# Optimization experiments

Measured on AMD Instinct MI355X. Metric: run time of the kernel, lower is better.

The kernel has to match this reference:

```python
import jax, jax.numpy as jnp
import numpy as np

N_HEADS = 8

def setup_inputs() -> dict:
    key = jax.random.key(0)
    k1, k2, k3 = jax.random.split(key, 3)
    B, T, C = 16, 1024, 512
    x = jax.random.normal(k1, (B, T, C), dtype=jnp.float32)
    Wqkv = jax.random.normal(k2, (C, 3 * C), dtype=jnp.float32) * (1.0 / np.sqrt(C))
    Wout = jax.random.normal(k3, (C, C), dtype=jnp.float32) * (1.0 / np.sqrt(C))
    return {"x": x, "Wqkv": Wqkv, "Wout": Wout}

def reference(x, Wqkv, Wout):
    B, T, C = x.shape
    H = N_HEADS
    Dh = C // H
    scale = 1.0 / (Dh ** 0.5)
    # qkv projection: [B,T,3,H,Dh] -> q,k,v each [B,H,T,Dh]
    qkv = (x @ Wqkv).reshape(B, T, 3, H, Dh)
    q = jnp.transpose(qkv[:, :, 0], (0, 2, 1, 3))
    k = jnp.transpose(qkv[:, :, 1], (0, 2, 1, 3))
    v = jnp.transpose(qkv[:, :, 2], (0, 2, 1, 3))
    att = jnp.einsum('bhqd,bhkd->bhqk', q, k) * scale  # [B,H,T,T]
    causal = jnp.tril(jnp.ones((T, T), dtype=bool))
    att = jnp.where(causal, att, -jnp.inf)
    att = jax.nn.softmax(att, axis=-1)
    y = jnp.einsum('bhqk,bhkd->bhqd', att, v)  # [B,H,T,Dh]
    y = jnp.transpose(y, (0, 2, 1, 3)).reshape(B, T, C)
    return y @ Wout
```

## Files before the change

kernel.cpp:

```cpp
#include <hip/hip_runtime.h>
#include <hip/hip_bf16.h>

typedef __bf16 bf16;
typedef __bf16 bf16x4 __attribute__((ext_vector_type(4)));
typedef __bf16 bf16x8 __attribute__((ext_vector_type(8)));
typedef float  f32x4  __attribute__((ext_vector_type(4)));

#define BB 16
#define TT 1024
#define CC 512
#define HH 8
#define DH 64

#define QSCALE 0.18033688011112042f
#define RESCALE_THR 10.0f

__device__ __forceinline__ void gload16(const void* gsrc, void* ldst) {
    __builtin_amdgcn_global_load_lds(
        (const __attribute__((address_space(1))) void*)gsrc,
        (__attribute__((address_space(3))) void*)ldst, 16, 0, 0);
}

__device__ __forceinline__ f32x4 mfma16(bf16x8 a, bf16x8 b, f32x4 c) {
    return __builtin_amdgcn_mfma_f32_16x16x32_bf16(a, b, c, 0, 0, 0);
}

__global__ __launch_bounds__(256)
void k_prep(const float* __restrict__ x, const float* __restrict__ wqkv,
            const float* __restrict__ wout,
            bf16* __restrict__ xb, bf16* __restrict__ wqt, bf16* __restrict__ wot)
{
    const int stride = gridDim.x * blockDim.x;
    const int i0 = blockIdx.x * blockDim.x + threadIdx.x;
    const int NX4 = BB * TT * CC / 4;
    for (int i = i0; i < NX4; i += stride) {
        float4 v = *(const float4*)(x + (size_t)i * 4);
        bf16x4 o = { (bf16)v.x, (bf16)v.y, (bf16)v.z, (bf16)v.w };
        *(bf16x4*)(xb + (size_t)i * 4) = o;
    }
    const int NQ = CC * 3 * CC;
    for (int i = i0; i < NQ; i += stride) {
        int k = i / (3 * CC), n = i - k * (3 * CC);
        wqt[(size_t)n * CC + k] = (bf16)wqkv[i];
    }
    const int NO = CC * CC;
    for (int i = i0; i < NO; i += stride) {
        int k = i / CC, n = i - k * CC;
        wot[(size_t)n * CC + k] = (bf16)wout[i];
    }
}

__global__ __launch_bounds__(512)
void k_attn(const bf16* __restrict__ qg, const bf16* __restrict__ kg,
            const bf16* __restrict__ vtg, bf16* __restrict__ yb)
{
    __shared__ __align__(16) bf16 sK[2][32 * 72];
    __shared__ __align__(16) bf16 sV[2][64 * 40];
    __shared__ __align__(16) bf16 sP[8][16 * 40];
    const int tid = threadIdx.x, w = tid >> 6, lane = tid & 63;
    const int l15 = lane & 15, l4 = lane >> 4;

    const int bid = blockIdx.x;
    const int xcd = bid & 7;
    const int j   = bid >> 3;
    const int bh  = xcd * 16 + (j >> 2);
    const int qp  = j & 3;

    const bf16* Q  = qg  + (size_t)bh * TT * DH;
    const bf16* Kp = kg  + (size_t)bh * TT * DH;
    const bf16* Vt = vtg + (size_t)bh * DH * TT;
    const int b = bh >> 3, h = bh & 7;

    const bool kstage = (tid < 256);
    const int ks_row = tid >> 3;
    const int ks_col = (tid & 7) * 8;
    const int t2 = tid & 255;
    const int vs_row = t2 >> 2;
    const int vs_col = (t2 & 3) * 8;

    bf16* myP = &sP[w][0];
    const f32x4 zero = {0.f, 0.f, 0.f, 0.f};

    for (int up = 0; up < 2; ++up) {
        const int qblk = up ? (7 - qp) : qp;
        const int qb   = qblk * 128 + w * 16;
        const int nt   = (qblk + 1) * 4;

        bf16x8 qf[2];
#pragma unroll
        for (int kk = 0; kk < 2; ++kk)
            qf[kk] = *(const bf16x8*)(Q + (size_t)(qb + l15) * DH + kk * 32 + l4 * 8);

        f32x4 y[4];
        float m_ = -1e30f, lp_ = 0.f;
#pragma unroll
        for (int dj = 0; dj < 4; ++dj) y[dj] = zero;

        if (kstage) {
            uint4 k0 = *(const uint4*)(Kp + (size_t)ks_row * DH + ks_col);
            *(uint4*)(&sK[0][ks_row * 72 + ks_col]) = k0;
        } else {
            uint4 v0 = *(const uint4*)(Vt + (size_t)vs_row * TT + vs_col);
            *(uint4*)(&sV[0][vs_row * 40 + vs_col]) = v0;
        }
        __syncthreads();

        for (int t = 0; t < nt; ++t) {
            const int t0 = t * 32;
            const int cur = t & 1, nxt = cur ^ 1;
            const bool more = (t + 1 < nt);
            uint4 sreg;
            if (more) {
                sreg = kstage
                    ? *(const uint4*)(Kp + (size_t)(t0 + 32 + ks_row) * DH + ks_col)
                    : *(const uint4*)(Vt + (size_t)vs_row * TT + t0 + 32 + vs_col);
            }

            if (t0 < qb + 16) {
                bf16x8 kf[2][2];
#pragma unroll
                for (int nj = 0; nj < 2; ++nj) {
                    const int row = nj * 16 + l15;
#pragma unroll
                    for (int kk = 0; kk < 2; ++kk)
                        kf[nj][kk] = *(const bf16x8*)(&sK[cur][row * 72 + ((kk << 2) | l4) * 8]);
                }
                f32x4 s[2];
#pragma unroll
                for (int nj = 0; nj < 2; ++nj) {
                    f32x4 a = mfma16(kf[nj][0], qf[0], zero);
                    s[nj] = mfma16(kf[nj][1], qf[1], a);
                }
                if (t0 + 32 > qb) {
#pragma unroll
                    for (int nj = 0; nj < 2; ++nj)
#pragma unroll
                        for (int rg = 0; rg < 4; ++rg)
                            if (t0 + nj * 16 + l4 * 4 + rg > qb + l15)
                                s[nj][rg] = -1e30f;
                }
                float mx = fmaxf(fmaxf(fmaxf(s[0][0], s[0][1]), fmaxf(s[0][2], s[0][3])),
                                 fmaxf(fmaxf(s[1][0], s[1][1]), fmaxf(s[1][2], s[1][3])));
                mx = fmaxf(mx, __shfl_xor(mx, 16));
                mx = fmaxf(mx, __shfl_xor(mx, 32));
                if (__any(mx > m_ + RESCALE_THR)) {
                    float mnew = fmaxf(m_, mx);
                    float corr = exp2f(m_ - mnew);
                    lp_ *= corr;
                    float cr[4];
#pragma unroll
                    for (int rg = 0; rg < 4; ++rg)
                        cr[rg] = __shfl(corr, ((lane >> 4) << 2) | rg);
#pragma unroll
                    for (int dj = 0; dj < 4; ++dj)
#pragma unroll
                        for (int rg = 0; rg < 4; ++rg) y[dj][rg] *= cr[rg];
                    m_ = mnew;
                }
                bf16x4 pk0, pk1;
#pragma unroll
                for (int rg = 0; rg < 4; ++rg) {
                    float p0 = exp2f(s[0][rg] - m_);
                    float p1 = exp2f(s[1][rg] - m_);
                    lp_ += p0 + p1;
                    pk0[rg] = (bf16)p0;
                    pk1[rg] = (bf16)p1;
                }
                *(bf16x4*)(myP + l15 * 40 + l4 * 4)      = pk0;
                *(bf16x4*)(myP + l15 * 40 + 16 + l4 * 4) = pk1;

                bf16x8 pa = *(const bf16x8*)(myP + l15 * 40 + l4 * 8);
                bf16x8 vf[4];
#pragma unroll
                for (int dj = 0; dj < 4; ++dj)
                    vf[dj] = *(const bf16x8*)(&sV[cur][(dj * 16 + l15) * 40 + l4 * 8]);
#pragma unroll
                for (int dj = 0; dj < 4; ++dj)
                    y[dj] = mfma16(pa, vf[dj], y[dj]);
            }

            if (more) {
                if (kstage) *(uint4*)(&sK[nxt][ks_row * 72 + ks_col]) = sreg;
                else        *(uint4*)(&sV[nxt][vs_row * 40 + vs_col]) = sreg;
            }
            __syncthreads();
        }

        lp_ += __shfl_xor(lp_, 16);
        lp_ += __shfl_xor(lp_, 32);
#pragma unroll
        for (int rg = 0; rg < 4; ++rg) {
            float inv = 1.0f / __shfl(lp_, ((lane >> 4) << 2) | rg);
            int rr = qb + l4 * 4 + rg;
#pragma unroll
            for (int dj = 0; dj < 4; ++dj) {
                int cc = h * DH + dj * 16 + l15;
                yb[((size_t)b * TT + rr) * CC + cc] = (bf16)(y[dj][rg] * inv);
            }
        }
        __syncthreads();
    }
}

template<int MODE>
__global__ __launch_bounds__(256)
void k_gemm_bt(const bf16* __restrict__ A, const bf16* __restrict__ Bt,
               int M, int N, int K,
               float* __restrict__ outF,
               bf16* __restrict__ qb, bf16* __restrict__ kb, bf16* __restrict__ vtb)
{
    __shared__ bf16 sA[2 * 128 * 32];
    __shared__ bf16 sB[2 * 128 * 32];
    const int tid  = threadIdx.x;
    const int wid  = tid >> 6;
    const int lane = tid & 63;
    const int l15  = lane & 15, l4 = lane >> 4;

    const int cpx = gridDim.x >> 3;
    const int bid = (blockIdx.x & 7) * cpx + (blockIdx.x >> 3);

    const int nNt = N >> 7;
    const int mt  = bid / nNt;
    const int nt  = bid - mt * nNt;
    const int m0  = mt << 7, n0 = nt << 7;
    const int wr  = (wid >> 1) * 64, wc = (wid & 1) * 64;

    f32x4 zero = {0.f, 0.f, 0.f, 0.f};
    f32x4 acc[4][4];
#pragma unroll
    for (int i = 0; i < 4; ++i)
#pragma unroll
        for (int j = 0; j < 4; ++j) acc[i][j] = zero;

    int srow[4], scol[4], soff[4];
#pragma unroll
    for (int c = 0; c < 4; ++c) {
        const int cc = wid * 4 + c;
        srow[c] = (cc & 7) * 16 + (lane >> 2);
        scol[c] = (cc >> 3) * 32 + (lane & 3) * 8;
        soff[c] = cc * 512;
    }

    for (int k0 = 0; k0 < K; k0 += 64) {
#pragma unroll
        for (int c = 0; c < 4; ++c)
            gload16(A  + (size_t)(m0 + srow[c]) * K + k0 + scol[c], sA + soff[c]);
#pragma unroll
        for (int c = 0; c < 4; ++c)
            gload16(Bt + (size_t)(n0 + srow[c]) * K + k0 + scol[c], sB + soff[c]);
        __syncthreads();
        bf16x8 af[4][2], bfr[4][2];
#pragma unroll
        for (int kk = 0; kk < 2; ++kk) {
#pragma unroll
            for (int i = 0; i < 4; ++i)
                af[i][kk] = *(const bf16x8*)(sA + kk * 4096 + (wr + i * 16 + l15) * 32 + l4 * 8);
#pragma unroll
            for (int j = 0; j < 4; ++j)
                bfr[j][kk] = *(const bf16x8*)(sB + kk * 4096 + (wc + j * 16 + l15) * 32 + l4 * 8);
        }
#pragma unroll
        for (int kk = 0; kk < 2; ++kk)
#pragma unroll
            for (int i = 0; i < 4; ++i)
#pragma unroll
                for (int j = 0; j < 4; ++j)
                    acc[i][j] = mfma16(bfr[j][kk], af[i][kk], acc[i][j]);
        __syncthreads();
    }

#pragma unroll
    for (int i = 0; i < 4; ++i) {
        const int rm = m0 + wr + i * 16 + l15;
#pragma unroll
        for (int j = 0; j < 4; ++j) {
            const int cn0 = n0 + wc + j * 16 + l4 * 4;
            if (MODE == 0) {
                *(f32x4*)(&outF[(size_t)rm * N + cn0]) = acc[i][j];
            } else {
                int b = rm >> 10, t = rm & 1023;
                int s = cn0 >> 9, h = (cn0 >> 6) & 7, d0 = cn0 & 63;
                size_t bh = (size_t)(b * HH + h);
                if (s == 0) {
                    bf16x4 o = { (bf16)(acc[i][j][0] * QSCALE), (bf16)(acc[i][j][1] * QSCALE),
                                 (bf16)(acc[i][j][2] * QSCALE), (bf16)(acc[i][j][3] * QSCALE) };
                    *(bf16x4*)(qb + (bh * TT + t) * DH + d0) = o;
                } else if (s == 1) {
                    bf16x4 o = { (bf16)acc[i][j][0], (bf16)acc[i][j][1],
                                 (bf16)acc[i][j][2], (bf16)acc[i][j][3] };
                    *(bf16x4*)(kb + (bh * TT + t) * DH + d0) = o;
                } else {
#pragma unroll
                    for (int rg = 0; rg < 4; ++rg)
                        vtb[(bh * DH + d0 + rg) * TT + t] = (bf16)acc[i][j][rg];
                }
            }
        }
    }
}

extern "C" void kernel_launch(void* const* d_in, const int* in_sizes, int n_in,
                              void* d_out, int out_size, void* d_ws, size_t ws_size,
                              hipStream_t stream)
{
    const float* x    = (const float*)d_in[0];
    const float* wqkv = (const float*)d_in[1];
    const float* wout = (const float*)d_in[2];
    float* out = (float*)d_out;

    const size_t NX = (size_t)BB * TT * CC;
    bf16* p   = (bf16*)d_ws;
    bf16* Xb  = p;  p += NX;
    bf16* Wqt = p;  p += (size_t)(3 * CC) * CC;
    bf16* Wot = p;  p += (size_t)CC * CC;
    bf16* Qb  = p;  p += NX;
    bf16* Kb  = p;  p += NX;
    bf16* Vtb = p;  p += NX;
    bf16* Yb  = Xb;

    k_prep<<<2048, 256, 0, stream>>>(x, wqkv, wout, Xb, Wqt, Wot);

    k_gemm_bt<1><<<(BB * TT / 128) * (3 * CC / 128), 256, 0, stream>>>(
        Xb, Wqt, BB * TT, 3 * CC, CC, nullptr, Qb, Kb, Vtb);

    k_attn<<<512, 512, 0, stream>>>(Qb, Kb, Vtb, Yb);

    k_gemm_bt<0><<<(BB * TT / 128) * (CC / 128), 256, 0, stream>>>(
        Yb, Wot, BB * TT, CC, CC, out, nullptr, nullptr, nullptr);
}
```

Before: 123.2 us.

## Unroll attention K/V tile loop by two with deeper register prefetch

Restructures the causal attention inner loop into a two-iteration unrolled body with two prefetch registers. Global loads for the K/V tile are now issued two tiles ahead, and the LDS buffer indices become compile-time constants. The aim is to hide more global-load latency and drop per-iteration buffer-index arithmetic. In exchange it uses more registers and relies on nt being even (nt=(qblk+1)*4 always is).

```diff
diff --git a/kernel.cpp b/kernel.cpp
--- a/kernel.cpp
+++ b/kernel.cpp
@@ -96,94 +96,99 @@
 #pragma unroll
         for (int dj = 0; dj < 4; ++dj) y[dj] = zero;
 
-        if (kstage) {
-            uint4 k0 = *(const uint4*)(Kp + (size_t)ks_row * DH + ks_col);
-            *(uint4*)(&sK[0][ks_row * 72 + ks_col]) = k0;
-        } else {
-            uint4 v0 = *(const uint4*)(Vt + (size_t)vs_row * TT + vs_col);
-            *(uint4*)(&sV[0][vs_row * 40 + vs_col]) = v0;
-        }
+        auto step = [&](int cbuf, int t0) {
+            bf16x8 kf[2][2];
+#pragma unroll
+            for (int nj = 0; nj < 2; ++nj) {
+                const int row = nj * 16 + l15;
+#pragma unroll
+                for (int kk = 0; kk < 2; ++kk)
+                    kf[nj][kk] = *(const bf16x8*)(&sK[cbuf][row * 72 + ((kk << 2) | l4) * 8]);
+            }
+            f32x4 s[2];
+#pragma unroll
+            for (int nj = 0; nj < 2; ++nj) {
+                f32x4 a = mfma16(kf[nj][0], qf[0], zero);
+                s[nj] = mfma16(kf[nj][1], qf[1], a);
+            }
+            if (t0 + 32 > qb) {
+#pragma unroll
+                for (int nj = 0; nj < 2; ++nj)
+#pragma unroll
+                    for (int rg = 0; rg < 4; ++rg)
+                        if (t0 + nj * 16 + l4 * 4 + rg > qb + l15)
+                            s[nj][rg] = -1e30f;
+            }
+            float mx = fmaxf(fmaxf(fmaxf(s[0][0], s[0][1]), fmaxf(s[0][2], s[0][3])),
+                             fmaxf(fmaxf(s[1][0], s[1][1]), fmaxf(s[1][2], s[1][3])));
+            mx = fmaxf(mx, __shfl_xor(mx, 16));
+            mx = fmaxf(mx, __shfl_xor(mx, 32));
+            if (__any(mx > m_ + RESCALE_THR)) {
+                float mnew = fmaxf(m_, mx);
+                float corr = exp2f(m_ - mnew);
+                lp_ *= corr;
+                float cr[4];
+#pragma unroll
+                for (int rg = 0; rg < 4; ++rg)
+                    cr[rg] = __shfl(corr, ((lane >> 4) << 2) | rg);
+#pragma unroll
+                for (int dj = 0; dj < 4; ++dj)
+#pragma unroll
+                    for (int rg = 0; rg < 4; ++rg) y[dj][rg] *= cr[rg];
+                m_ = mnew;
+            }
+            bf16x4 pk0, pk1;
+#pragma unroll
+            for (int rg = 0; rg < 4; ++rg) {
+                float p0 = exp2f(s[0][rg] - m_);
+                float p1 = exp2f(s[1][rg] - m_);
+                lp_ += p0 + p1;
+                pk0[rg] = (bf16)p0;
+                pk1[rg] = (bf16)p1;
+            }
+            *(bf16x4*)(myP + l15 * 40 + l4 * 4)      = pk0;
+            *(bf16x4*)(myP + l15 * 40 + 16 + l4 * 4) = pk1;
+
+            bf16x8 pa = *(const bf16x8*)(myP + l15 * 40 + l4 * 8);
+            bf16x8 vf[4];
+#pragma unroll
+            for (int dj = 0; dj < 4; ++dj)
+                vf[dj] = *(const bf16x8*)(&sV[cbuf][(dj * 16 + l15) * 40 + l4 * 8]);
+#pragma unroll
+            for (int dj = 0; dj < 4; ++dj)
+                y[dj] = mfma16(pa, vf[dj], y[dj]);
+        };
+
+        auto gload = [&](int tile) -> uint4 {
+            return kstage
+                ? *(const uint4*)(Kp + (size_t)(tile * 32 + ks_row) * DH + ks_col)
+                : *(const uint4*)(Vt + (size_t)vs_row * TT + tile * 32 + vs_col);
+        };
+        auto swrite = [&](int buf, uint4 v) {
+            if (kstage) *(uint4*)(&sK[buf][ks_row * 72 + ks_col]) = v;
+            else        *(uint4*)(&sV[buf][vs_row * 40 + vs_col]) = v;
+        };
+
+        uint4 sregA, sregB;
+        swrite(0, gload(0));
+        sregA = gload(1);
         __syncthreads();
 
-        for (int t = 0; t < nt; ++t) {
-            const int t0 = t * 32;
-            const int cur = t & 1, nxt = cur ^ 1;
-            const bool more = (t + 1 < nt);
-            uint4 sreg;
-            if (more) {
-                sreg = kstage
-                    ? *(const uint4*)(Kp + (size_t)(t0 + 32 + ks_row) * DH + ks_col)
-                    : *(const uint4*)(Vt + (size_t)vs_row * TT + t0 + 32 + vs_col);
-            }
-
-            if (t0 < qb + 16) {
-                bf16x8 kf[2][2];
-#pragma unroll
-                for (int nj = 0; nj < 2; ++nj) {
-                    const int row = nj * 16 + l15;
-#pragma unroll
-                    for (int kk = 0; kk < 2; ++kk)
-                        kf[nj][kk] = *(const bf16x8*)(&sK[cur][row * 72 + ((kk << 2) | l4) * 8]);
-                }
-                f32x4 s[2];
-#pragma unroll
-                for (int nj = 0; nj < 2; ++nj) {
-                    f32x4 a = mfma16(kf[nj][0], qf[0], zero);
-                    s[nj] = mfma16(kf[nj][1], qf[1], a);
-                }
-                if (t0 + 32 > qb) {
-#pragma unroll
-                    for (int nj = 0; nj < 2; ++nj)
-#pragma unroll
-                        for (int rg = 0; rg < 4; ++rg)
-                            if (t0 + nj * 16 + l4 * 4 + rg > qb + l15)
-                                s[nj][rg] = -1e30f;
-                }
-                float mx = fmaxf(fmaxf(fmaxf(s[0][0], s[0][1]), fmaxf(s[0][2], s[0][3])),
-                                 fmaxf(fmaxf(s[1][0], s[1][1]), fmaxf(s[1][2], s[1][3])));
-                mx = fmaxf(mx, __shfl_xor(mx, 16));
-                mx = fmaxf(mx, __shfl_xor(mx, 32));
-                if (__any(mx > m_ + RESCALE_THR)) {
-                    float mnew = fmaxf(m_, mx);
-                    float corr = exp2f(m_ - mnew);
-                    lp_ *= corr;
-                    float cr[4];
-#pragma unroll
-                    for (int rg = 0; rg < 4; ++rg)
-                        cr[rg] = __shfl(corr, ((lane >> 4) << 2) | rg);
-#pragma unroll
-                    for (int dj = 0; dj < 4; ++dj)
-#pragma unroll
-                        for (int rg = 0; rg < 4; ++rg) y[dj][rg] *= cr[rg];
-                    m_ = mnew;
-                }
-                bf16x4 pk0, pk1;
-#pragma unroll
-                for (int rg = 0; rg < 4; ++rg) {
-                    float p0 = exp2f(s[0][rg] - m_);
-                    float p1 = exp2f(s[1][rg] - m_);
-                    lp_ += p0 + p1;
-                    pk0[rg] = (bf16)p0;
-                    pk1[rg] = (bf16)p1;
-                }
-                *(bf16x4*)(myP + l15 * 40 + l4 * 4)      = pk0;
-                *(bf16x4*)(myP + l15 * 40 + 16 + l4 * 4) = pk1;
-
-                bf16x8 pa = *(const bf16x8*)(myP + l15 * 40 + l4 * 8);
-                bf16x8 vf[4];
-#pragma unroll
-                for (int dj = 0; dj < 4; ++dj)
-                    vf[dj] = *(const bf16x8*)(&sV[cur][(dj * 16 + l15) * 40 + l4 * 8]);
-#pragma unroll
-                for (int dj = 0; dj < 4; ++dj)
-                    y[dj] = mfma16(pa, vf[dj], y[dj]);
-            }
-
-            if (more) {
-                if (kstage) *(uint4*)(&sK[nxt][ks_row * 72 + ks_col]) = sreg;
-                else        *(uint4*)(&sV[nxt][vs_row * 40 + vs_col]) = sreg;
-            }
-            __syncthreads();
+        for (int t = 0; t < nt; t += 2) {
+            {
+                const int t0 = t * 32;
+                if (t + 2 < nt) sregB = gload(t + 2);
+                if (t0 < qb + 16) step(0, t0);
+                swrite(1, sregA);
+                __syncthreads();
+            }
+            {
+                const int t0 = (t + 1) * 32;
+                if (t + 3 < nt) sregA = gload(t + 3);
+                if (t0 < qb + 16) step(1, t0);
+                if (t + 2 < nt) swrite(0, sregB);
+                __syncthreads();
+            }
         }
 
         lp_ += __shfl_xor(lp_, 16);
```

After: 125.4 us. Within noise of the previous version (+1.8%).
